# Kernel optimization log

Measured on AMD Instinct MI355X. Metric: run time of the kernel, lower is better.

## Reference

```python
import jax, jax.numpy as jnp
import numpy as np

NUM_NODES, WINDOW, DIM, B = 50000, 8, 256, 8192


def setup_inputs() -> dict:
    key = jax.random.key(0)
    k1, k2, k3, k4, k5, k6 = jax.random.split(key, 6)
    return {
        "bank": jax.random.normal(k1, (NUM_NODES, WINDOW, DIM), dtype=jnp.float32),
        "timestamps": jax.random.uniform(k2, (NUM_NODES, WINDOW), dtype=jnp.float32),
        "neighbor_repr": jax.random.normal(k3, (B, DIM), dtype=jnp.float32),
        "t": jax.random.uniform(k4, (B,), dtype=jnp.float32) * 1000.0,
        "ptr": jax.random.randint(k5, (NUM_NODES,), 0, 1000000, dtype=jnp.int64) if jax.config.jax_enable_x64 else jax.random.randint(k5, (NUM_NODES,), 0, 1000000, dtype=jnp.int32),
        "idx": jax.random.randint(k6, (B,), 0, NUM_NODES, dtype=jnp.int32),
    }


def reference(bank, timestamps, neighbor_repr, t, ptr, idx):
    """Vectorized equivalent of NeighborhoodEvolutionBank.write().

    The torch loop writes batch elements sequentially: the k-th occurrence of a
    node index within the batch lands in slot (ptr[node] + k) % window, and ptr
    is bumped once per occurrence. We reproduce that by computing, for each
    batch element, its rank among earlier duplicates of the same index.
    """
    window = bank.shape[1]
    # rank[bi] = number of j < bi with idx[j] == idx[bi]  (B x B, B=8192 -> 64M bool, fine)
    eq = idx[:, None] == idx[None, :]
    rank = jnp.sum(jnp.tril(eq, k=-1), axis=1).astype(ptr.dtype)  # [B]
    slot = (ptr[idx] + rank) % window                              # [B]

    bank_new = bank.at[idx, slot].set(neighbor_repr)               # fused scatter write
    ts_new = timestamps.at[idx, slot].set(t.astype(timestamps.dtype))
    ptr_new = ptr.at[idx].add(1)
    return bank_new, ts_new, ptr_new
```

## Files before the change

### kernel.cpp

```cpp
#include <hip/hip_runtime.h>

#define NUM_NODES 50000
#define WINDOW 8
#define DIM 256
#define BATCH 8192
#define NROWS (NUM_NODES * WINDOW)
#define ROW4  (DIM / 4)
#define BANK4 ((long)NROWS * ROW4)
#define WINNER_INTS (NROWS / 2)

typedef float f4 __attribute__((ext_vector_type(4)));


__global__ void __launch_bounds__(256)
init_kernel(int* __restrict__ ws) {
    int i = blockIdx.x * 256 + threadIdx.x;
    if (i < NUM_NODES) ws[i] = 0;
    else if (i < NUM_NODES + WINNER_INTS) ws[i] = 0xFFFFFFFF;
    else if (i == NUM_NODES + WINNER_INTS) ws[i] = 0;
}

__global__ void __launch_bounds__(256)
count_kernel(const int* __restrict__ idx, int* __restrict__ count) {
    int bi = blockIdx.x * 256 + threadIdx.x;
    if (bi < BATCH) atomicAdd(&count[idx[bi]], 1);
}

__global__ void __launch_bounds__(256)
classify_kernel(const int* __restrict__ idx, const int* __restrict__ ptr,
                const int* __restrict__ count, short* __restrict__ winner,
                int* __restrict__ duplist, int* __restrict__ dupN,
                float* __restrict__ out_ptr) {
    int i = blockIdx.x * 256 + threadIdx.x;
    if (i < NUM_NODES) out_ptr[i] = (float)(ptr[i] + count[i]);
    if (i < BATCH) {
        int node = idx[i];
        int c    = count[node];
        if (c == 1) winner[node * WINDOW + (ptr[node] & (WINDOW - 1))] = (short)i;
        else        duplist[atomicAdd(dupN, 1)] = i;
    }
}

__global__ void __launch_bounds__(256)
dup_rank_kernel(const int* __restrict__ idx, const int* __restrict__ ptr,
                const int* __restrict__ count,
                const int* __restrict__ duplist, const int* __restrict__ dupN,
                short* __restrict__ winner) {
    __shared__ int spos [BATCH];
    __shared__ int snode[BATCH];
    int n = *dupN;
    for (int k = threadIdx.x; k < n; k += 256) {
        int p = duplist[k];
        spos [k] = p;
        snode[k] = idx[p];
    }
    __syncthreads();

    int k = blockIdx.x * 256 + threadIdx.x;
    if (k >= n) return;
    int p    = spos[k];
    int node = snode[k];
    int rank = 0;
    for (int m = 0; m < n; ++m)
        rank += (spos[m] < p && snode[m] == node);

    if (rank >= count[node] - WINDOW)
        winner[node * WINDOW + ((ptr[node] + rank) & (WINDOW - 1))] = (short)p;
}

__global__ void __launch_bounds__(256)
copy_kernel(const f4* __restrict__ bank4, const float* __restrict__ ts,
            const f4* __restrict__ nrep4, const float* __restrict__ t,
            const short* __restrict__ winner,
            f4* __restrict__ out_bank4, float* __restrict__ out_ts) {
    long gid = (long)blockIdx.x * 256 + threadIdx.x;
    int  row = (int)(gid >> 6);
    int  off = (int)(gid & 63);
    int  w   = winner[row];
    f4 v;
    if (w >= 0) v = nrep4[(long)w * ROW4 + off];
    else        v = __builtin_nontemporal_load(&bank4[gid]);
    __builtin_nontemporal_store(v, &out_bank4[gid]);
    if (off == 0) out_ts[row] = (w >= 0) ? t[w] : ts[row];
}

extern "C" void kernel_launch(void* const* d_in, const int* in_sizes, int n_in,
                              void* d_out, int out_size, void* d_ws, size_t ws_size,
                              hipStream_t stream) {
    const float* bank       = (const float*)d_in[0];
    const float* timestamps = (const float*)d_in[1];
    const float* nrep       = (const float*)d_in[2];
    const float* t          = (const float*)d_in[3];
    const int*   ptr        = (const int*)  d_in[4];
    const int*   idx        = (const int*)  d_in[5];

    float* out_bank = (float*)d_out;
    float* out_ts   = out_bank + (size_t)NUM_NODES * WINDOW * DIM;
    float* out_ptr  = out_ts   + (size_t)NUM_NODES * WINDOW;

    int*   count   = (int*)d_ws;
    short* winner  = (short*)(count + NUM_NODES);
    int*   dupN    = count + NUM_NODES + WINNER_INTS;
    int*   duplist = dupN + 1;

    const int initN = NUM_NODES + WINNER_INTS + 1;
    init_kernel    <<<(initN + 255) / 256, 256, 0, stream>>>((int*)d_ws);
    count_kernel   <<<(BATCH + 255) / 256, 256, 0, stream>>>(idx, count);
    classify_kernel<<<(NUM_NODES + 255) / 256, 256, 0, stream>>>(idx, ptr, count,
                                                winner, duplist, dupN, out_ptr);
    dup_rank_kernel<<<(BATCH + 255) / 256, 256, 0, stream>>>(idx, ptr, count,
                                                duplist, dupN, winner);

    copy_kernel<<<(int)(BANK4 / 256), 256, 0, stream>>>(
        (const f4*)bank, timestamps, (const f4*)nrep, t, winner,
        (f4*)out_bank, out_ts);
}
```

Before: 265.1 us.

## Use memset init, int winner map, and grid-stride copy without nontemporal hints

Replaces the custom init kernel with two hipMemsetAsync calls and widens the winner map from short to int, which doubles its size. The one-thread-per-float4 copy kernel becomes a grid-stride loop over 2048 blocks using plain loads and stores instead of nontemporal builtins. The aim is to cut launch overhead and per-block scheduling cost. The trade-offs are losing the cache-bypass hints on a roughly 400 MB streaming copy and the extra traffic from the larger winner array.

```diff
diff --git a/kernel.cpp b/kernel.cpp
--- a/kernel.cpp
+++ b/kernel.cpp
@@ -7,18 +7,7 @@
 #define NROWS (NUM_NODES * WINDOW)
 #define ROW4  (DIM / 4)
 #define BANK4 ((long)NROWS * ROW4)
-#define WINNER_INTS (NROWS / 2)
 
-typedef float f4 __attribute__((ext_vector_type(4)));
-
-
-__global__ void __launch_bounds__(256)
-init_kernel(int* __restrict__ ws) {
-    int i = blockIdx.x * 256 + threadIdx.x;
-    if (i < NUM_NODES) ws[i] = 0;
-    else if (i < NUM_NODES + WINNER_INTS) ws[i] = 0xFFFFFFFF;
-    else if (i == NUM_NODES + WINNER_INTS) ws[i] = 0;
-}
 
 __global__ void __launch_bounds__(256)
 count_kernel(const int* __restrict__ idx, int* __restrict__ count) {
@@ -28,16 +17,17 @@
 
 __global__ void __launch_bounds__(256)
 classify_kernel(const int* __restrict__ idx, const int* __restrict__ ptr,
-                const int* __restrict__ count, short* __restrict__ winner,
+                const int* __restrict__ count, int* __restrict__ winner,
                 int* __restrict__ duplist, int* __restrict__ dupN,
                 float* __restrict__ out_ptr) {
     int i = blockIdx.x * 256 + threadIdx.x;
     if (i < NUM_NODES) out_ptr[i] = (float)(ptr[i] + count[i]);
     if (i < BATCH) {
         int node = idx[i];
-        int c    = count[node];
-        if (c == 1) winner[node * WINDOW + (ptr[node] & (WINDOW - 1))] = (short)i;
-        else        duplist[atomicAdd(dupN, 1)] = i;
+        if (count[node] == 1)
+            winner[node * WINDOW + (ptr[node] & (WINDOW - 1))] = i;
+        else
+            duplist[atomicAdd(dupN, 1)] = i;
     }
 }
 
@@ -45,7 +35,7 @@
 dup_rank_kernel(const int* __restrict__ idx, const int* __restrict__ ptr,
                 const int* __restrict__ count,
                 const int* __restrict__ duplist, const int* __restrict__ dupN,
-                short* __restrict__ winner) {
+                int* __restrict__ winner) {
     __shared__ int spos [BATCH];
     __shared__ int snode[BATCH];
     int n = *dupN;
@@ -65,23 +55,26 @@
         rank += (spos[m] < p && snode[m] == node);
 
     if (rank >= count[node] - WINDOW)
-        winner[node * WINDOW + ((ptr[node] + rank) & (WINDOW - 1))] = (short)p;
+        winner[node * WINDOW + ((ptr[node] + rank) & (WINDOW - 1))] = p;
 }
 
 __global__ void __launch_bounds__(256)
-copy_kernel(const f4* __restrict__ bank4, const float* __restrict__ ts,
-            const f4* __restrict__ nrep4, const float* __restrict__ t,
-            const short* __restrict__ winner,
-            f4* __restrict__ out_bank4, float* __restrict__ out_ts) {
-    long gid = (long)blockIdx.x * 256 + threadIdx.x;
-    int  row = (int)(gid >> 6);
-    int  off = (int)(gid & 63);
-    int  w   = winner[row];
-    f4 v;
-    if (w >= 0) v = nrep4[(long)w * ROW4 + off];
-    else        v = __builtin_nontemporal_load(&bank4[gid]);
-    __builtin_nontemporal_store(v, &out_bank4[gid]);
-    if (off == 0) out_ts[row] = (w >= 0) ? t[w] : ts[row];
+fused_copy_kernel(const float4* __restrict__ bank4,
+                  const float*  __restrict__ ts,
+                  const float4* __restrict__ nrep4,
+                  const float*  __restrict__ t,
+                  const int*    __restrict__ winner,
+                  float4* __restrict__ out_bank4,
+                  float*  __restrict__ out_ts) {
+    const long nth = (long)gridDim.x * 256;
+    for (long i = (long)blockIdx.x * 256 + threadIdx.x; i < BANK4; i += nth) {
+        int  row = (int)(i >> 6);
+        int  w   = winner[row];
+        float4 v = (w >= 0) ? nrep4[(long)w * ROW4 + (i & 63)] : bank4[i];
+        out_bank4[i] = v;
+        if ((i & 63) == 0)
+            out_ts[row] = (w >= 0) ? t[w] : ts[row];
+    }
 }
 
 extern "C" void kernel_launch(void* const* d_in, const int* in_sizes, int n_in,
@@ -98,20 +91,21 @@
     float* out_ts   = out_bank + (size_t)NUM_NODES * WINDOW * DIM;
     float* out_ptr  = out_ts   + (size_t)NUM_NODES * WINDOW;
 
-    int*   count   = (int*)d_ws;
-    short* winner  = (short*)(count + NUM_NODES);
-    int*   dupN    = count + NUM_NODES + WINNER_INTS;
-    int*   duplist = dupN + 1;
+    int* count   = (int*)d_ws;
+    int* dupN    = count + NUM_NODES;
+    int* duplist = dupN + 1;
+    int* winner  = duplist + BATCH;
 
-    const int initN = NUM_NODES + WINNER_INTS + 1;
-    init_kernel    <<<(initN + 255) / 256, 256, 0, stream>>>((int*)d_ws);
+    hipMemsetAsync(count, 0, (NUM_NODES + 1) * sizeof(int), stream);
+    hipMemsetAsync(winner, 0xFF, (size_t)NROWS * sizeof(int), stream);
+
     count_kernel   <<<(BATCH + 255) / 256, 256, 0, stream>>>(idx, count);
     classify_kernel<<<(NUM_NODES + 255) / 256, 256, 0, stream>>>(idx, ptr, count,
                                                 winner, duplist, dupN, out_ptr);
     dup_rank_kernel<<<(BATCH + 255) / 256, 256, 0, stream>>>(idx, ptr, count,
                                                 duplist, dupN, winner);
 
-    copy_kernel<<<(int)(BANK4 / 256), 256, 0, stream>>>(
-        (const f4*)bank, timestamps, (const f4*)nrep, t, winner,
-        (f4*)out_bank, out_ts);
+    fused_copy_kernel<<<2048, 256, 0, stream>>>(
+        (const float4*)bank, timestamps, (const float4*)nrep, t, winner,
+        (float4*)out_bank, out_ts);
 }
```

Measured after the change: 280.2 us. 1.06x slower.
